# Kernel optimization log

Measured on AMD Instinct MI355X. Metric: run time of the kernel, lower is better.

## Reference

```python
import jax, jax.numpy as jnp
import numpy as np

N_QUBITS = 12
N_LAYERS = 4
BATCH = 1024


def _apply_1q(state, G, w, n):
    # state: (b, 2**n) complex; G: (2,2) shared or (b,2,2) batched gate on wire w
    b = state.shape[0]
    st = state.reshape(b, 2**w, 2, 2**(n - w - 1))
    if G.ndim == 3:
        out = jnp.einsum('bij,bljr->blir', G, st)
    else:
        out = jnp.einsum('ij,bljr->blir', G, st)
    return out.reshape(b, -1)


def _apply_cnot(state, c, t, n):
    # CNOT with control c, target t; reshape so both wire axes are explicit
    b = state.shape[0]
    q0, q1 = (c, t) if c < t else (t, c)
    st = state.reshape(b, 2**q0, 2, 2**(q1 - q0 - 1), 2, 2**(n - q1 - 1))
    if c < t:
        # control axis = 2; flip target axis in the control=1 slice
        out = jnp.stack([st[:, :, 0], jnp.flip(st[:, :, 1], axis=3)], axis=2)
    else:
        # control axis = 4; target axis sits at position 2 of the slice
        out = jnp.stack([st[:, :, :, :, 0], jnp.flip(st[:, :, :, :, 1], axis=2)], axis=4)
    return out.reshape(b, -1)


def _vqc_forward(x, weights):
    b, n = x.shape
    L = weights.shape[0]
    state = jnp.zeros((b, 2**n), jnp.complex64).at[:, 0].set(1.0)
    # AngleEmbedding (default rotation='X'): RX(x[:, w]) on wire w, batched gates
    half = x.astype(jnp.float32) * 0.5
    c, s = jnp.cos(half), jnp.sin(half)
    for w in range(n):
        G = jnp.stack([jnp.stack([c[:, w] + 0j, -1j * s[:, w]], -1),
                       jnp.stack([-1j * s[:, w], c[:, w] + 0j], -1)], -2)  # (b,2,2)
        state = _apply_1q(state, G, w, n)
    # StronglyEntanglingLayers: per layer, Rot(phi,theta,omega) on each wire,
    # then ring of CNOTs with range r = l % (n-1) + 1
    for l in range(L):
        for w in range(n):
            phi, theta, omega = weights[l, w, 0], weights[l, w, 1], weights[l, w, 2]
            ct, sn = jnp.cos(theta * 0.5), jnp.sin(theta * 0.5)
            ep = jnp.exp(0.5j * (phi + omega))
            em = jnp.exp(-0.5j * (phi + omega))
            ed = jnp.exp(0.5j * (phi - omega))
            edc = jnp.exp(-0.5j * (phi - omega))
            # Rot = RZ(omega) @ RY(theta) @ RZ(phi)
            G = jnp.stack([jnp.stack([em * ct, -ed * sn]),
                           jnp.stack([edc * sn, ep * ct])])  # (2,2)
            state = _apply_1q(state, G, w, n)
        r = l % (n - 1) + 1
        for w in range(n):
            state = _apply_cnot(state, w, (w + r) % n, n)
    # <Z_w> = sum over basis states of probs * (+1 if bit w == 0 else -1)
    probs = state.real**2 + state.imag**2
    evs = []
    for w in range(n):
        p = probs.reshape(b, 2**w, 2, -1)
        evs.append(p[:, :, 0, :].sum(axis=(1, 2)) - p[:, :, 1, :].sum(axis=(1, 2)))
    return jnp.stack(evs, axis=1)  # (b, n_qubits)


def setup_inputs() -> dict:
    key = jax.random.key(0)
    k1, k2 = jax.random.split(key)
    x = jax.random.uniform(k1, (BATCH, N_QUBITS), jnp.float32) * np.float32(np.pi)
    weights = jax.random.normal(k2, (N_LAYERS, N_QUBITS, 3), jnp.float32)
    return {"x": x, "weights": weights}


def reference(x, weights):
    return _vqc_forward(x, weights)
```

## Files before the change

kernel.cpp:

```cpp
#include <hip/hip_runtime.h>

#define NQ 12
#define NL 4
typedef __attribute__((ext_vector_type(2))) float f32x2;


__device__ __forceinline__ f32x2 cmul(f32x2 a, f32x2 b) {
    f32x2 r; r.x = a.x*b.x - a.y*b.y; r.y = a.x*b.y + a.y*b.x; return r;
}

__device__ __forceinline__ int SW(int i) {
    return i ^ ((((i >> 4) ^ (i >> 8)) & 7) << 1);
}

template<int P>
__device__ __forceinline__ void ry16(f32x2 (&v)[16], float ct, float sn) {
#pragma unroll
    for (int r0 = 0; r0 < 16; ++r0) {
        if (!(r0 & (1 << P))) {
            const int r1 = r0 | (1 << P);
            const f32x2 a0 = v[r0], a1 = v[r1];
            v[r0] = ct*a0 - sn*a1;
            v[r1] = sn*a0 + ct*a1;
        }
    }
}

__device__ __forceinline__ void ry4grp(f32x2 (&v)[16], const f32x2* rc) {
    const f32x2 c0 = rc[0], c1 = rc[1], c2 = rc[2], c3 = rc[3];
    ry16<3>(v, c0.x, c0.y);
    ry16<2>(v, c1.x, c1.y);
    ry16<1>(v, c2.x, c2.y);
    ry16<0>(v, c3.x, c3.y);
}

__device__ __forceinline__ void diag16(f32x2 (&v)[16], const f32x2* tab, f32x2 tc) {
#pragma unroll
    for (int r = 0; r < 16; ++r)
        v[r] = cmul(v[r], cmul(tc, tab[r]));
}

__device__ constexpr int foldG(int rho, int r) {
    int g = 0;
    if (rho == 1) {
        if (r & 1) g ^= 0xC01; if (r & 2) g ^= 0x003;
        if (r & 4) g ^= 0x006; if (r & 8) g ^= 0x00C;
    } else if (rho == 2) {
        if (r & 1) g ^= 0x501; if (r & 2) g ^= 0xA02;
        if (r & 4) g ^= 0x005; if (r & 8) g ^= 0x00A;
    } else {
        if (r & 1) g ^= 0x241; if (r & 2) g ^= 0x482;
        if (r & 4) g ^= 0x904; if (r & 8) g ^= 0x009;
    }
    return g;
}

template<int RHO>
__device__ __forceinline__ void readCA(f32x2 (&v)[16], const f32x2* buf, int t) {
    int F;
    if constexpr (RHO == 1) F = (t << 4) ^ ((t & 127) << 3) ^ ((t >> 7) << 10);
    else if constexpr (RHO == 2) F = (t << 4) ^ ((t & 255) << 2);
    else F = (t << 4) ^ ((t & 255) << 1);
#pragma unroll
    for (int r = 0; r < 16; ++r)
        v[r] = buf[SW(F ^ foldG(RHO, r))];
}

__global__ __launch_bounds__(256) void vqc_kernel(
    const float* __restrict__ x,
    const float* __restrict__ wts,
    float* __restrict__ out)
{
    __shared__ alignas(16) f32x2 buf[4096];
    __shared__ alignas(16) f32x2 dtabP[NL][16];
    __shared__ alignas(16) f32x2 dtabW[3][16];
    __shared__ alignas(16) f32x2 rcs[NL * NQ];
    __shared__ float wtsL[NL * NQ * 3];
    __shared__ float red[4][NQ];

    const int t = threadIdx.x;
    const int b = blockIdx.x;

    if (t < NL * NQ * 3) wtsL[t] = wts[t];
    if (t < 112) {
        const int tb = t >> 4, e = t & 15;
        float ang = 0.f;
        if (tb < NL) {
#pragma unroll
            for (int j = 0; j < 4; ++j)
                ang += (((e >> j) & 1) ? 0.5f : -0.5f) * wts[(tb*NQ + (11-j))*3 + 0];
            float s, c; __sincosf(ang, &s, &c);
            f32x2 tv = {c, s}; dtabP[tb][e] = tv;
        } else {
            const int l = tb - NL;
#pragma unroll
            for (int j = 0; j < 4; ++j)
                ang += (((e >> j) & 1) ? 0.5f : -0.5f) * wts[(l*NQ + (3-j))*3 + 2];
            float s, c; __sincosf(ang, &s, &c);
            f32x2 tv = {c, s}; dtabW[l][e] = tv;
        }
    }
    if (t < NL * NQ) {
        float s, c; __sincosf(0.5f * wts[t*3 + 1], &s, &c);
        f32x2 tv = {c, s}; rcs[t] = tv;
    }
    __syncthreads();

    float cw[NQ], sw[NQ];
#pragma unroll
    for (int w = 0; w < NQ; ++w)
        __sincosf(0.5f * x[b*NQ + w], &sw[w], &cw[w]);
    float lm = 1.f;
#pragma unroll
    for (int k = 0; k < 8; ++k)
        lm *= ((t >> k) & 1) ? sw[7-k] : cw[7-k];
    const int pt = __popc(t) & 3;
    float pre[4], pim[4];
#pragma unroll
    for (int q = 0; q < 4; ++q) {
        const int kk = (pt + q) & 3;
        pre[q] = (kk == 0) ? 1.f : ((kk == 2) ? -1.f : 0.f);
        pim[q] = (kk == 1) ? -1.f : ((kk == 3) ? 1.f : 0.f);
    }
    f32x2 v[16];
#pragma unroll
    for (int r = 0; r < 16; ++r) {
        float m = lm;
        m *= (r & 1) ? sw[11] : cw[11];
        m *= (r & 2) ? sw[10] : cw[10];
        m *= (r & 4) ? sw[9]  : cw[9];
        m *= (r & 8) ? sw[8]  : cw[8];
        const int pc = __popc(r) & 3;
        v[r].x = m * pre[pc];
        v[r].y = m * pim[pc];
    }

#pragma unroll 1
    for (int l = 0; l < NL; ++l) {
        float angP = 0.f;
#pragma unroll
        for (int k = 0; k < 8; ++k)
            angP += (((t >> k) & 1) ? 0.5f : -0.5f) * wtsL[(l*NQ + (7-k))*3 + 0];
        float sp, cp; __sincosf(angP, &sp, &cp);
        f32x2 tcP = {cp, sp};
        diag16(v, dtabP[l], tcP);

        ry4grp(v, &rcs[l*NQ + 8]);

        __syncthreads();
        {
            float4* b4 = (float4*)buf;
            const int base = t << 4;
#pragma unroll
            for (int r = 0; r < 16; r += 2) {
                const int a = SW(base | r);
                b4[a >> 1] = make_float4(v[r].x, v[r].y, v[r+1].x, v[r+1].y);
            }
        }
        __syncthreads();
        {
            const int hi = (t & 0xF0) << 4, lo = t & 15;
#pragma unroll
            for (int r = 0; r < 16; ++r)
                v[r] = buf[SW(hi | (r << 4) | lo)];
        }

        ry4grp(v, &rcs[l*NQ + 4]);

        __syncthreads();
        {
            const int hi = (t & 0xF0) << 4, lo = t & 15;
#pragma unroll
            for (int r = 0; r < 16; ++r)
                buf[SW(hi | (r << 4) | lo)] = v[r];
        }
        __syncthreads();
#pragma unroll
        for (int r = 0; r < 16; ++r)
            v[r] = buf[SW((r << 8) | t)];

        ry4grp(v, &rcs[l*NQ + 0]);

        if (l == NL - 1) break;

        float angW = 0.f;
#pragma unroll
        for (int k = 0; k < 8; ++k)
            angW += (((t >> k) & 1) ? 0.5f : -0.5f) * wtsL[(l*NQ + (11-k))*3 + 2];
        float so, co; __sincosf(angW, &so, &co);
        f32x2 tcW = {co, so};
        diag16(v, dtabW[l], tcW);

        __syncthreads();
#pragma unroll
        for (int r = 0; r < 16; ++r)
            buf[SW((r << 8) | t)] = v[r];
        __syncthreads();
        if (l == 0)      readCA<1>(v, buf, t);
        else if (l == 1) readCA<2>(v, buf, t);
        else             readCA<3>(v, buf, t);
    }

    float S0 = 0.f, S8 = 0.f, S4 = 0.f, S2 = 0.f, S1 = 0.f;
#pragma unroll
    for (int r = 0; r < 16; ++r) {
        const float p = v[r].x*v[r].x + v[r].y*v[r].y;
        S0 += p;
        S8 += (r & 8) ? -p : p;
        S4 += (r & 4) ? -p : p;
        S2 += (r & 2) ? -p : p;
        S1 += (r & 1) ? -p : p;
    }
    const float g88 = (__popc(t & 0x88) & 1) ? -1.f : 1.f;
    const float g44 = (__popc(t & 0x44) & 1) ? -1.f : 1.f;
    const float g22 = (__popc(t & 0x22) & 1) ? -1.f : 1.f;
    const float g11 = (__popc(t & 0x11) & 1) ? -1.f : 1.f;
    const float g80 = (t & 0x80) ? -1.f : 1.f;
    const float g40 = (t & 0x40) ? -1.f : 1.f;
    const float g20 = (t & 0x20) ? -1.f : 1.f;
    const float g10 = (t & 0x10) ? -1.f : 1.f;

    float ev[NQ];
    ev[0] = g88 * S0;  ev[1] = g44 * S0;  ev[2]  = g22 * S0;  ev[3]  = g11 * S0;
    ev[4] = g80 * S8;  ev[5] = g40 * S4;  ev[6]  = g20 * S2;  ev[7]  = g10 * S1;
    ev[8] = g88 * S8;  ev[9] = g44 * S4;  ev[10] = g22 * S2;  ev[11] = g11 * S1;

#pragma unroll
    for (int w = 0; w < NQ; ++w)
#pragma unroll
        for (int off = 32; off; off >>= 1)
            ev[w] += __shfl_xor(ev[w], off, 64);
    if ((t & 63) == 0) {
#pragma unroll
        for (int w = 0; w < NQ; ++w) red[t >> 6][w] = ev[w];
    }
    __syncthreads();
    if (t < NQ) out[b*NQ + t] = red[0][t] + red[1][t] + red[2][t] + red[3][t];
}

extern "C" void kernel_launch(void* const* d_in, const int* in_sizes, int n_in,
                              void* d_out, int out_size, void* d_ws, size_t ws_size,
                              hipStream_t stream) {
    const float* x   = (const float*)d_in[0];
    const float* wts = (const float*)d_in[1];
    float* out = (float*)d_out;
    const int nb = in_sizes[0] / NQ;
    vqc_kernel<<<dim3(nb), dim3(256), 0, stream>>>(x, wts, out);
}
```

Baseline: 43.10 us.

## Process two batch samples per block and factor RZ diagonal into per-bit phases

Each block now simulates two batch elements with one shared 4096-entry LDS buffer, so the per-block weight setup is amortized and the two state vectors' gate arithmetic can interleave. The 16-entry diagonal phase tables are replaced by four per-bit phase factors plus a scalar offset, applied as successive complex multiplies. Weights are read directly from global memory instead of being staged in shared memory. In exchange there are twice as many barriers per block (serialized permutes through one buffer), higher register pressure from two 16-element complex arrays, half as many blocks, and an odd batch size would drop the last sample.

```diff
diff --git a/kernel.cpp b/kernel.cpp
--- a/kernel.cpp
+++ b/kernel.cpp
@@ -34,10 +34,18 @@
     ry16<0>(v, c3.x, c3.y);
 }
 
-__device__ __forceinline__ void diag16(f32x2 (&v)[16], const f32x2* tab, f32x2 tc) {
-#pragma unroll
-    for (int r = 0; r < 16; ++r)
-        v[r] = cmul(v[r], cmul(tc, tab[r]));
+__device__ __forceinline__ void diag_rz(f32x2 (&v)[16], f32x2 tc, const f32x2* fz) {
+    const f32x2 f0 = fz[0], f1 = fz[1], f2 = fz[2], f3 = fz[3];
+#pragma unroll
+    for (int r = 0; r < 16; ++r) v[r] = cmul(v[r], tc);
+#pragma unroll
+    for (int r = 8; r < 16; ++r) v[r] = cmul(v[r], f0);
+#pragma unroll
+    for (int r = 0; r < 16; ++r) if (r & 4) v[r] = cmul(v[r], f1);
+#pragma unroll
+    for (int r = 0; r < 16; ++r) if (r & 2) v[r] = cmul(v[r], f2);
+#pragma unroll
+    for (int r = 0; r < 16; ++r) if (r & 1) v[r] = cmul(v[r], f3);
 }
 
 __device__ constexpr int foldG(int rho, int r) {
@@ -66,54 +74,41 @@
         v[r] = buf[SW(F ^ foldG(RHO, r))];
 }
 
-__global__ __launch_bounds__(256) void vqc_kernel(
-    const float* __restrict__ x,
-    const float* __restrict__ wts,
-    float* __restrict__ out)
-{
-    __shared__ alignas(16) f32x2 buf[4096];
-    __shared__ alignas(16) f32x2 dtabP[NL][16];
-    __shared__ alignas(16) f32x2 dtabW[3][16];
-    __shared__ alignas(16) f32x2 rcs[NL * NQ];
-    __shared__ float wtsL[NL * NQ * 3];
-    __shared__ float red[4][NQ];
-
-    const int t = threadIdx.x;
-    const int b = blockIdx.x;
-
-    if (t < NL * NQ * 3) wtsL[t] = wts[t];
-    if (t < 112) {
-        const int tb = t >> 4, e = t & 15;
-        float ang = 0.f;
-        if (tb < NL) {
-#pragma unroll
-            for (int j = 0; j < 4; ++j)
-                ang += (((e >> j) & 1) ? 0.5f : -0.5f) * wts[(tb*NQ + (11-j))*3 + 0];
-            float s, c; __sincosf(ang, &s, &c);
-            f32x2 tv = {c, s}; dtabP[tb][e] = tv;
-        } else {
-            const int l = tb - NL;
-#pragma unroll
-            for (int j = 0; j < 4; ++j)
-                ang += (((e >> j) & 1) ? 0.5f : -0.5f) * wts[(l*NQ + (3-j))*3 + 2];
-            float s, c; __sincosf(ang, &s, &c);
-            f32x2 tv = {c, s}; dtabW[l][e] = tv;
-        }
-    }
-    if (t < NL * NQ) {
-        float s, c; __sincosf(0.5f * wts[t*3 + 1], &s, &c);
-        f32x2 tv = {c, s}; rcs[t] = tv;
-    }
-    __syncthreads();
-
+__device__ __forceinline__ void permA_write(const f32x2 (&v)[16], f32x2* buf, int t) {
+    float4* b4 = (float4*)buf;
+    const int base = t << 4;
+#pragma unroll
+    for (int r = 0; r < 16; r += 2) {
+        const int a = SW(base | r);
+        b4[a >> 1] = make_float4(v[r].x, v[r].y, v[r+1].x, v[r+1].y);
+    }
+}
+__device__ __forceinline__ void permB_read(f32x2 (&v)[16], const f32x2* buf, int t) {
+    const int hi = (t & 0xF0) << 4, lo = t & 15;
+#pragma unroll
+    for (int r = 0; r < 16; ++r) v[r] = buf[SW(hi | (r << 4) | lo)];
+}
+__device__ __forceinline__ void permB_write(const f32x2 (&v)[16], f32x2* buf, int t) {
+    const int hi = (t & 0xF0) << 4, lo = t & 15;
+#pragma unroll
+    for (int r = 0; r < 16; ++r) buf[SW(hi | (r << 4) | lo)] = v[r];
+}
+__device__ __forceinline__ void permC_read(f32x2 (&v)[16], const f32x2* buf, int t) {
+#pragma unroll
+    for (int r = 0; r < 16; ++r) v[r] = buf[SW((r << 8) | t)];
+}
+__device__ __forceinline__ void permC_write(const f32x2 (&v)[16], f32x2* buf, int t) {
+#pragma unroll
+    for (int r = 0; r < 16; ++r) buf[SW((r << 8) | t)] = v[r];
+}
+
+__device__ __forceinline__ void embed(f32x2 (&v)[16], const float* __restrict__ xr, int t) {
     float cw[NQ], sw[NQ];
 #pragma unroll
-    for (int w = 0; w < NQ; ++w)
-        __sincosf(0.5f * x[b*NQ + w], &sw[w], &cw[w]);
+    for (int w = 0; w < NQ; ++w) __sincosf(0.5f * xr[w], &sw[w], &cw[w]);
     float lm = 1.f;
 #pragma unroll
-    for (int k = 0; k < 8; ++k)
-        lm *= ((t >> k) & 1) ? sw[7-k] : cw[7-k];
+    for (int k = 0; k < 8; ++k) lm *= ((t >> k) & 1) ? sw[7-k] : cw[7-k];
     const int pt = __popc(t) & 3;
     float pre[4], pim[4];
 #pragma unroll
@@ -122,7 +117,6 @@
         pre[q] = (kk == 0) ? 1.f : ((kk == 2) ? -1.f : 0.f);
         pim[q] = (kk == 1) ? -1.f : ((kk == 3) ? 1.f : 0.f);
     }
-    f32x2 v[16];
 #pragma unroll
     for (int r = 0; r < 16; ++r) {
         float m = lm;
@@ -134,73 +128,9 @@
         v[r].x = m * pre[pc];
         v[r].y = m * pim[pc];
     }
-
-#pragma unroll 1
-    for (int l = 0; l < NL; ++l) {
-        float angP = 0.f;
-#pragma unroll
-        for (int k = 0; k < 8; ++k)
-            angP += (((t >> k) & 1) ? 0.5f : -0.5f) * wtsL[(l*NQ + (7-k))*3 + 0];
-        float sp, cp; __sincosf(angP, &sp, &cp);
-        f32x2 tcP = {cp, sp};
-        diag16(v, dtabP[l], tcP);
-
-        ry4grp(v, &rcs[l*NQ + 8]);
-
-        __syncthreads();
-        {
-            float4* b4 = (float4*)buf;
-            const int base = t << 4;
-#pragma unroll
-            for (int r = 0; r < 16; r += 2) {
-                const int a = SW(base | r);
-                b4[a >> 1] = make_float4(v[r].x, v[r].y, v[r+1].x, v[r+1].y);
-            }
-        }
-        __syncthreads();
-        {
-            const int hi = (t & 0xF0) << 4, lo = t & 15;
-#pragma unroll
-            for (int r = 0; r < 16; ++r)
-                v[r] = buf[SW(hi | (r << 4) | lo)];
-        }
-
-        ry4grp(v, &rcs[l*NQ + 4]);
-
-        __syncthreads();
-        {
-            const int hi = (t & 0xF0) << 4, lo = t & 15;
-#pragma unroll
-            for (int r = 0; r < 16; ++r)
-                buf[SW(hi | (r << 4) | lo)] = v[r];
-        }
-        __syncthreads();
-#pragma unroll
-        for (int r = 0; r < 16; ++r)
-            v[r] = buf[SW((r << 8) | t)];
-
-        ry4grp(v, &rcs[l*NQ + 0]);
-
-        if (l == NL - 1) break;
-
-        float angW = 0.f;
-#pragma unroll
-        for (int k = 0; k < 8; ++k)
-            angW += (((t >> k) & 1) ? 0.5f : -0.5f) * wtsL[(l*NQ + (11-k))*3 + 2];
-        float so, co; __sincosf(angW, &so, &co);
-        f32x2 tcW = {co, so};
-        diag16(v, dtabW[l], tcW);
-
-        __syncthreads();
-#pragma unroll
-        for (int r = 0; r < 16; ++r)
-            buf[SW((r << 8) | t)] = v[r];
-        __syncthreads();
-        if (l == 0)      readCA<1>(v, buf, t);
-        else if (l == 1) readCA<2>(v, buf, t);
-        else             readCA<3>(v, buf, t);
-    }
-
+}
+
+__device__ __forceinline__ void meas(const f32x2 (&v)[16], float (&ev)[NQ], int t) {
     float S0 = 0.f, S8 = 0.f, S4 = 0.f, S2 = 0.f, S1 = 0.f;
 #pragma unroll
     for (int r = 0; r < 16; ++r) {
@@ -219,23 +149,131 @@
     const float g40 = (t & 0x40) ? -1.f : 1.f;
     const float g20 = (t & 0x20) ? -1.f : 1.f;
     const float g10 = (t & 0x10) ? -1.f : 1.f;
-
-    float ev[NQ];
     ev[0] = g88 * S0;  ev[1] = g44 * S0;  ev[2]  = g22 * S0;  ev[3]  = g11 * S0;
     ev[4] = g80 * S8;  ev[5] = g40 * S4;  ev[6]  = g20 * S2;  ev[7]  = g10 * S1;
     ev[8] = g88 * S8;  ev[9] = g44 * S4;  ev[10] = g22 * S2;  ev[11] = g11 * S1;
-
-#pragma unroll
-    for (int w = 0; w < NQ; ++w)
-#pragma unroll
-        for (int off = 32; off; off >>= 1)
-            ev[w] += __shfl_xor(ev[w], off, 64);
+}
+
+__global__ __launch_bounds__(256) void vqc_kernel(
+    const float* __restrict__ x,
+    const float* __restrict__ wts,
+    float* __restrict__ out)
+{
+    __shared__ alignas(16) f32x2 buf[4096];
+    __shared__ alignas(16) f32x2 rcs[NL * NQ];
+    __shared__ alignas(16) f32x2 rzP[NL][4];
+    __shared__ alignas(16) f32x2 rzW[3][4];
+    __shared__ float offs[8];
+    __shared__ float red[2][4][NQ];
+
+    const int t  = threadIdx.x;
+    const int b0 = blockIdx.x * 2, b1 = b0 + 1;
+
+    if (t < NL * NQ) {
+        float s, c; __sincosf(0.5f * wts[t*3 + 1], &s, &c);
+        f32x2 tv = {c, s}; rcs[t] = tv;
+    } else if (t < 64) {
+        const int u = t - 48, l = u >> 2, j = u & 3;
+        float s, c; __sincosf(wts[(l*NQ + 8 + j)*3 + 0], &s, &c);
+        f32x2 tv = {c, s}; rzP[l][j] = tv;
+    } else if (t < 76) {
+        const int u = t - 64, l = u >> 2, j = u & 3;
+        float s, c; __sincosf(wts[(l*NQ + j)*3 + 2], &s, &c);
+        f32x2 tv = {c, s}; rzW[l][j] = tv;
+    } else if (t < 80) {
+        const int l = t - 76;
+        float s = 0.f;
+#pragma unroll
+        for (int j = 0; j < 4; ++j) s += wts[(l*NQ + 8 + j)*3 + 0];
+        offs[l] = -0.5f * s;
+    } else if (t < 83) {
+        const int l = t - 80;
+        float s = 0.f;
+#pragma unroll
+        for (int j = 0; j < 4; ++j) s += wts[(l*NQ + j)*3 + 2];
+        offs[4 + l] = -0.5f * s;
+    }
+
+    f32x2 v0[16], v1[16];
+    embed(v0, x + b0*NQ, t);
+    embed(v1, x + b1*NQ, t);
+    __syncthreads();
+
+#pragma unroll 1
+    for (int l = 0; l < NL; ++l) {
+        float aP = offs[l];
+#pragma unroll
+        for (int k = 0; k < 8; ++k)
+            aP += (((t >> k) & 1) ? 0.5f : -0.5f) * wts[(l*NQ + (7-k))*3 + 0];
+        float sp, cp; __sincosf(aP, &sp, &cp);
+        f32x2 tcP = {cp, sp};
+        diag_rz(v0, tcP, rzP[l]);
+        diag_rz(v1, tcP, rzP[l]);
+        ry4grp(v0, &rcs[l*NQ + 8]);
+        ry4grp(v1, &rcs[l*NQ + 8]);
+
+        __syncthreads(); permA_write(v0, buf, t);
+        __syncthreads(); permB_read(v0, buf, t);
+        __syncthreads(); permA_write(v1, buf, t);
+        __syncthreads(); permB_read(v1, buf, t);
+        ry4grp(v0, &rcs[l*NQ + 4]);
+        ry4grp(v1, &rcs[l*NQ + 4]);
+
+        __syncthreads(); permB_write(v0, buf, t);
+        __syncthreads(); permC_read(v0, buf, t);
+        __syncthreads(); permB_write(v1, buf, t);
+        __syncthreads(); permC_read(v1, buf, t);
+        ry4grp(v0, &rcs[l*NQ + 0]);
+        ry4grp(v1, &rcs[l*NQ + 0]);
+
+        if (l == NL - 1) break;
+
+        float aW = offs[4 + l];
+#pragma unroll
+        for (int k = 0; k < 8; ++k)
+            aW += (((t >> k) & 1) ? 0.5f : -0.5f) * wts[(l*NQ + (11-k))*3 + 2];
+        float so, co; __sincosf(aW, &so, &co);
+        f32x2 tcW = {co, so};
+        diag_rz(v0, tcW, rzW[l]);
+        diag_rz(v1, tcW, rzW[l]);
+
+        __syncthreads(); permC_write(v0, buf, t);
+        __syncthreads();
+        if (l == 0)      readCA<1>(v0, buf, t);
+        else if (l == 1) readCA<2>(v0, buf, t);
+        else             readCA<3>(v0, buf, t);
+        __syncthreads(); permC_write(v1, buf, t);
+        __syncthreads();
+        if (l == 0)      readCA<1>(v1, buf, t);
+        else if (l == 1) readCA<2>(v1, buf, t);
+        else             readCA<3>(v1, buf, t);
+    }
+
+    float ev0[NQ], ev1[NQ];
+    meas(v0, ev0, t);
+    meas(v1, ev1, t);
+#pragma unroll
+    for (int w = 0; w < NQ; ++w) {
+#pragma unroll
+        for (int off = 32; off; off >>= 1) {
+            ev0[w] += __shfl_xor(ev0[w], off, 64);
+            ev1[w] += __shfl_xor(ev1[w], off, 64);
+        }
+    }
     if ((t & 63) == 0) {
 #pragma unroll
-        for (int w = 0; w < NQ; ++w) red[t >> 6][w] = ev[w];
+        for (int w = 0; w < NQ; ++w) {
+            red[0][t >> 6][w] = ev0[w];
+            red[1][t >> 6][w] = ev1[w];
+        }
     }
     __syncthreads();
-    if (t < NQ) out[b*NQ + t] = red[0][t] + red[1][t] + red[2][t] + red[3][t];
+    if (t < NQ)
+        out[b0*NQ + t] = red[0][0][t] + red[0][1][t] + red[0][2][t] + red[0][3][t];
+    else if (t >= 64 && t < 64 + NQ) {
+        const int w = t - 64;
+        out[b1*NQ + w] = red[1][0][w] + red[1][1][w] + red[1][2][w] + red[1][3][w];
+    }
 }
 
 extern "C" void kernel_launch(void* const* d_in, const int* in_sizes, int n_in,
@@ -244,6 +282,6 @@
     const float* x   = (const float*)d_in[0];
     const float* wts = (const float*)d_in[1];
     float* out = (float*)d_out;
-    const int nb = in_sizes[0] / NQ;
-    vqc_kernel<<<dim3(nb), dim3(256), 0, stream>>>(x, wts, out);
-}
+    const int nb2 = (in_sizes[0] / NQ) / 2;
+    vqc_kernel<<<dim3(nb2), dim3(256), 0, stream>>>(x, wts, out);
+}
```

After: 53.49 us. 1.24x slower.

## Halve block to 128 threads with 32 amplitudes each, DPP gate and fused CNOT exchange

Applied to the files above, without the earlier changes.

Each block now uses 128 threads holding 32 amplitudes per thread instead of 256 holding 16, so five wires are applied in registers per pass. One wire's rotation is done through a cross-lane DPP swap, and the CNOT ring permutation is fused with the next rotation during the shared-memory read. This cuts the number of shared-memory transposes and barriers per layer, and one barrier is replaced by a local lgkmcnt wait that relies on the write/read mapping staying within a wavefront. In exchange, register pressure rises and there are fewer threads per block.

```diff
diff --git a/kernel.cpp b/kernel.cpp
--- a/kernel.cpp
+++ b/kernel.cpp
@@ -9,14 +9,19 @@
     f32x2 r; r.x = a.x*b.x - a.y*b.y; r.y = a.x*b.y + a.y*b.x; return r;
 }
 
-__device__ __forceinline__ int SW(int i) {
-    return i ^ ((((i >> 4) ^ (i >> 8)) & 7) << 1);
+__host__ __device__ constexpr int SLc(int s) {
+    return s ^ ((((s >> 5) ^ (s >> 9)) & 15) << 1);
+}
+
+__device__ __forceinline__ float dppx1(float x) {
+    return __int_as_float(__builtin_amdgcn_mov_dpp(__float_as_int(x), 0xB1, 0xF, 0xF, true));
 }
 
 template<int P>
-__device__ __forceinline__ void ry16(f32x2 (&v)[16], float ct, float sn) {
-#pragma unroll
-    for (int r0 = 0; r0 < 16; ++r0) {
+__device__ __forceinline__ void ry32(f32x2 (&v)[32], f32x2 g) {
+    const float ct = g.x, sn = g.y;
+#pragma unroll
+    for (int r0 = 0; r0 < 32; ++r0) {
         if (!(r0 & (1 << P))) {
             const int r1 = r0 | (1 << P);
             const f32x2 a0 = v[r0], a1 = v[r1];
@@ -26,95 +31,124 @@
     }
 }
 
-__device__ __forceinline__ void ry4grp(f32x2 (&v)[16], const f32x2* rc) {
-    const f32x2 c0 = rc[0], c1 = rc[1], c2 = rc[2], c3 = rc[3];
-    ry16<3>(v, c0.x, c0.y);
-    ry16<2>(v, c1.x, c1.y);
-    ry16<1>(v, c2.x, c2.y);
-    ry16<0>(v, c3.x, c3.y);
-}
-
-__device__ __forceinline__ void diag16(f32x2 (&v)[16], const f32x2* tab, f32x2 tc) {
-#pragma unroll
-    for (int r = 0; r < 16; ++r)
-        v[r] = cmul(v[r], cmul(tc, tab[r]));
-}
-
-__device__ constexpr int foldG(int rho, int r) {
+__device__ __forceinline__ void diag32(f32x2 (&v)[32], f32x2 tc, const f32x2* f) {
+#pragma unroll
+    for (int r = 0; r < 32; ++r) v[r] = cmul(v[r], tc);
+#pragma unroll
+    for (int j = 0; j < 5; ++j) {
+        const f32x2 fj = f[j];
+#pragma unroll
+        for (int r = 0; r < 32; ++r)
+            if (r & (1 << j)) v[r] = cmul(v[r], fj);
+    }
+}
+
+template<int RHO>
+__device__ __forceinline__ constexpr int GmaskF(int r) {
     int g = 0;
-    if (rho == 1) {
-        if (r & 1) g ^= 0xC01; if (r & 2) g ^= 0x003;
-        if (r & 4) g ^= 0x006; if (r & 8) g ^= 0x00C;
-    } else if (rho == 2) {
-        if (r & 1) g ^= 0x501; if (r & 2) g ^= 0xA02;
-        if (r & 4) g ^= 0x005; if (r & 8) g ^= 0x00A;
+    if constexpr (RHO == 1) {
+        if (r & 1) g ^= 0xC01; if (r & 2) g ^= 0x003; if (r & 4) g ^= 0x006;
+        if (r & 8) g ^= 0x00C; if (r & 16) g ^= 0x018;
+        if ((r ^ (r >> 1)) & 1) g ^= 0x41;
+    } else if constexpr (RHO == 2) {
+        if (r & 1) g ^= 0x501; if (r & 2) g ^= 0xA02; if (r & 4) g ^= 0x005;
+        if (r & 8) g ^= 0x00A; if (r & 16) g ^= 0x014;
+        if ((r ^ (r >> 2)) & 1) g ^= 0x41;
     } else {
-        if (r & 1) g ^= 0x241; if (r & 2) g ^= 0x482;
-        if (r & 4) g ^= 0x904; if (r & 8) g ^= 0x009;
-    }
-    return g;
+        if (r & 1) g ^= 0x241; if (r & 2) g ^= 0x482; if (r & 4) g ^= 0x904;
+        if (r & 8) g ^= 0x009; if (r & 16) g ^= 0x012;
+        if ((r >> 3) & 1) g ^= 0x41;
+    }
+    return SLc(g);
 }
 
 template<int RHO>
-__device__ __forceinline__ void readCA(f32x2 (&v)[16], const f32x2* buf, int t) {
-    int F;
-    if constexpr (RHO == 1) F = (t << 4) ^ ((t & 127) << 3) ^ ((t >> 7) << 10);
-    else if constexpr (RHO == 2) F = (t << 4) ^ ((t & 255) << 2);
-    else F = (t << 4) ^ ((t & 255) << 1);
-#pragma unroll
-    for (int r = 0; r < 16; ++r)
-        v[r] = buf[SW(F ^ foldG(RHO, r))];
-}
-
-__global__ __launch_bounds__(256) void vqc_kernel(
+__device__ __forceinline__ void exchange_ring(f32x2 (&v)[32], const f32x2* buf, int t,
+    f32x2 cAa, f32x2 cBa, f32x2 cAb, f32x2 cBb)
+{
+    int T = 0;
+    if constexpr (RHO == 1) {
+        if (t & 64) T ^= 0xC00; if (t & 32) T ^= 0x600; if (t & 16) T ^= 0x300;
+        if (t & 8) T ^= 0x180;  if (t & 4) T ^= 0x0C0;  if (t & 2) T ^= 0x060;
+        if (t & 1) T ^= 0x030;
+        if (((t >> 1) ^ (t >> 2)) & 1) T ^= 0x41;
+    } else if constexpr (RHO == 2) {
+        if (t & 64) T ^= 0xA00; if (t & 32) T ^= 0x500; if (t & 16) T ^= 0x280;
+        if (t & 8) T ^= 0x140;  if (t & 4) T ^= 0x0A0;  if (t & 2) T ^= 0x050;
+        if (t & 1) T ^= 0x028;
+        if (((t >> 1) ^ (t >> 3)) & 1) T ^= 0x41;
+    } else {
+        if (t & 64) T ^= 0x900; if (t & 32) T ^= 0x480; if (t & 16) T ^= 0x240;
+        if (t & 8) T ^= 0x120;  if (t & 4) T ^= 0x090;  if (t & 2) T ^= 0x048;
+        if (t & 1) T ^= 0x024;
+        if (((t >> 1) ^ (t >> 4)) & 1) T ^= 0x41;
+    }
+    const int TT = SLc(T);
+#pragma unroll
+    for (int r = 0; r < 32; ++r) {
+        const int s0 = TT ^ GmaskF<RHO>(r);
+        const f32x2 a  = buf[s0];
+        const f32x2 bb = buf[s0 ^ 0x808];
+        const bool hb = (r >> (RHO - 1)) & 1;
+        const f32x2 cA = hb ? cAb : cAa;
+        const f32x2 cB = hb ? cBb : cBa;
+        v[r] = cmul(cA, a) + cmul(cB, bb);
+    }
+}
+
+__global__ __launch_bounds__(128) void vqc_kernel(
     const float* __restrict__ x,
     const float* __restrict__ wts,
     float* __restrict__ out)
 {
     __shared__ alignas(16) f32x2 buf[4096];
-    __shared__ alignas(16) f32x2 dtabP[NL][16];
-    __shared__ alignas(16) f32x2 dtabW[3][16];
     __shared__ alignas(16) f32x2 rcs[NL * NQ];
-    __shared__ float wtsL[NL * NQ * 3];
-    __shared__ float red[4][NQ];
+    __shared__ alignas(16) f32x2 fphi[NL][5];
+    __shared__ alignas(16) f32x2 fomg[3][5];
+    __shared__ f32x2 eo[3];
+    __shared__ float offp[NL], offo[3];
+    __shared__ float red[2][NQ];
 
     const int t = threadIdx.x;
     const int b = blockIdx.x;
 
-    if (t < NL * NQ * 3) wtsL[t] = wts[t];
-    if (t < 112) {
-        const int tb = t >> 4, e = t & 15;
-        float ang = 0.f;
-        if (tb < NL) {
-#pragma unroll
-            for (int j = 0; j < 4; ++j)
-                ang += (((e >> j) & 1) ? 0.5f : -0.5f) * wts[(tb*NQ + (11-j))*3 + 0];
-            float s, c; __sincosf(ang, &s, &c);
-            f32x2 tv = {c, s}; dtabP[tb][e] = tv;
-        } else {
-            const int l = tb - NL;
-#pragma unroll
-            for (int j = 0; j < 4; ++j)
-                ang += (((e >> j) & 1) ? 0.5f : -0.5f) * wts[(l*NQ + (3-j))*3 + 2];
-            float s, c; __sincosf(ang, &s, &c);
-            f32x2 tv = {c, s}; dtabW[l][e] = tv;
-        }
-    }
-    if (t < NL * NQ) {
+    if (t < 48) {
         float s, c; __sincosf(0.5f * wts[t*3 + 1], &s, &c);
         f32x2 tv = {c, s}; rcs[t] = tv;
-    }
-    __syncthreads();
+    } else if (t < 68) {
+        const int u = t - 48, l = u / 5, j = u % 5;
+        float s, c; __sincosf(wts[(l*NQ + 11 - j)*3 + 0], &s, &c);
+        f32x2 tv = {c, s}; fphi[l][j] = tv;
+    } else if (t < 83) {
+        const int u = t - 68, l = u / 5, j = u % 5;
+        float s, c; __sincosf(wts[(l*NQ + 5 - j)*3 + 2], &s, &c);
+        f32x2 tv = {c, s}; fomg[l][j] = tv;
+    } else if (t < 86) {
+        const int l = t - 83;
+        float s, c; __sincosf(0.5f * wts[(l*NQ + 0)*3 + 2], &s, &c);
+        f32x2 tv = {c, s}; eo[l] = tv;
+    } else if (t < 90) {
+        const int l = t - 86;
+        float s = 0.f;
+#pragma unroll
+        for (int w = 7; w <= 11; ++w) s += wts[(l*NQ + w)*3 + 0];
+        offp[l] = -0.5f * s;
+    } else if (t < 93) {
+        const int l = t - 90;
+        float s = 0.f;
+#pragma unroll
+        for (int w = 1; w <= 5; ++w) s += wts[(l*NQ + w)*3 + 2];
+        offo[l] = -0.5f * s;
+    }
 
     float cw[NQ], sw[NQ];
 #pragma unroll
-    for (int w = 0; w < NQ; ++w)
-        __sincosf(0.5f * x[b*NQ + w], &sw[w], &cw[w]);
+    for (int w = 0; w < NQ; ++w) __sincosf(0.5f * x[b*NQ + w], &sw[w], &cw[w]);
     float lm = 1.f;
 #pragma unroll
-    for (int k = 0; k < 8; ++k)
-        lm *= ((t >> k) & 1) ? sw[7-k] : cw[7-k];
-    const int pt = __popc(t) & 3;
+    for (int k = 0; k < 7; ++k)
+        lm *= ((t >> k) & 1) ? sw[6-k] : cw[6-k];
+    const int pt = __popc(t & 127) & 3;
     float pre[4], pim[4];
 #pragma unroll
     for (int q = 0; q < 4; ++q) {
@@ -122,108 +156,148 @@
         pre[q] = (kk == 0) ? 1.f : ((kk == 2) ? -1.f : 0.f);
         pim[q] = (kk == 1) ? -1.f : ((kk == 3) ? 1.f : 0.f);
     }
-    f32x2 v[16];
-#pragma unroll
-    for (int r = 0; r < 16; ++r) {
+    f32x2 v[32];
+#pragma unroll
+    for (int r = 0; r < 32; ++r) {
         float m = lm;
-        m *= (r & 1) ? sw[11] : cw[11];
-        m *= (r & 2) ? sw[10] : cw[10];
-        m *= (r & 4) ? sw[9]  : cw[9];
-        m *= (r & 8) ? sw[8]  : cw[8];
+        m *= (r & 1)  ? sw[11] : cw[11];
+        m *= (r & 2)  ? sw[10] : cw[10];
+        m *= (r & 4)  ? sw[9]  : cw[9];
+        m *= (r & 8)  ? sw[8]  : cw[8];
+        m *= (r & 16) ? sw[7]  : cw[7];
         const int pc = __popc(r) & 3;
         v[r].x = m * pre[pc];
         v[r].y = m * pim[pc];
     }
+    __syncthreads();
+
+    const int wA = (t << 5) ^ (((t ^ (t >> 4)) & 15) << 1);
+    const int jb = ((t & 64) << 5) | ((t & 1) << 5) | ((t >> 1) & 31);
+    const int rbase = SLc(jb);
+    const int wbase = SLc(jb ^ (((t >> 1) & 1) ? 0x41 : 0));
+    float4* const b4 = (float4*)buf;
 
 #pragma unroll 1
     for (int l = 0; l < NL; ++l) {
-        float angP = 0.f;
-#pragma unroll
-        for (int k = 0; k < 8; ++k)
-            angP += (((t >> k) & 1) ? 0.5f : -0.5f) * wtsL[(l*NQ + (7-k))*3 + 0];
-        float sp, cp; __sincosf(angP, &sp, &cp);
-        f32x2 tcP = {cp, sp};
-        diag16(v, dtabP[l], tcP);
-
-        ry4grp(v, &rcs[l*NQ + 8]);
-
-        __syncthreads();
         {
-            float4* b4 = (float4*)buf;
-            const int base = t << 4;
-#pragma unroll
-            for (int r = 0; r < 16; r += 2) {
-                const int a = SW(base | r);
-                b4[a >> 1] = make_float4(v[r].x, v[r].y, v[r+1].x, v[r+1].y);
-            }
-        }
-        __syncthreads();
+            float ang = offp[l];
+#pragma unroll
+            for (int k = 0; k < 7; ++k) {
+                const float a = 0.5f * wts[(l*NQ + (6-k))*3 + 0];
+                ang += ((t >> k) & 1) ? a : -a;
+            }
+            float s, c; __sincosf(ang, &s, &c);
+            f32x2 tc = {c, s};
+            diag32(v, tc, fphi[l]);
+        }
+        ry32<4>(v, rcs[l*NQ + 7]);  ry32<3>(v, rcs[l*NQ + 8]);
+        ry32<2>(v, rcs[l*NQ + 9]);  ry32<1>(v, rcs[l*NQ + 10]);
+        ry32<0>(v, rcs[l*NQ + 11]);
+
+#pragma unroll
+        for (int r = 0; r < 32; r += 2) {
+            const int sl = wA ^ r;
+            b4[sl >> 1] = make_float4(v[r].x, v[r].y, v[r+1].x, v[r+1].y);
+        }
+        asm volatile("s_waitcnt lgkmcnt(0)" ::: "memory");
+#pragma unroll
+        for (int r = 0; r < 32; ++r)
+            v[r] = buf[rbase ^ SLc(r << 6)];
+
+        ry32<4>(v, rcs[l*NQ + 1]);  ry32<3>(v, rcs[l*NQ + 2]);
+        ry32<2>(v, rcs[l*NQ + 3]);  ry32<1>(v, rcs[l*NQ + 4]);
+        ry32<0>(v, rcs[l*NQ + 5]);
+
         {
-            const int hi = (t & 0xF0) << 4, lo = t & 15;
-#pragma unroll
-            for (int r = 0; r < 16; ++r)
-                v[r] = buf[SW(hi | (r << 4) | lo)];
-        }
-
-        ry4grp(v, &rcs[l*NQ + 4]);
-
-        __syncthreads();
-        {
-            const int hi = (t & 0xF0) << 4, lo = t & 15;
-#pragma unroll
-            for (int r = 0; r < 16; ++r)
-                buf[SW(hi | (r << 4) | lo)] = v[r];
-        }
-        __syncthreads();
-#pragma unroll
-        for (int r = 0; r < 16; ++r)
-            v[r] = buf[SW((r << 8) | t)];
-
-        ry4grp(v, &rcs[l*NQ + 0]);
-
-        if (l == NL - 1) break;
-
-        float angW = 0.f;
-#pragma unroll
-        for (int k = 0; k < 8; ++k)
-            angW += (((t >> k) & 1) ? 0.5f : -0.5f) * wtsL[(l*NQ + (11-k))*3 + 2];
-        float so, co; __sincosf(angW, &so, &co);
-        f32x2 tcW = {co, so};
-        diag16(v, dtabW[l], tcW);
-
-        __syncthreads();
-#pragma unroll
-        for (int r = 0; r < 16; ++r)
-            buf[SW((r << 8) | t)] = v[r];
-        __syncthreads();
-        if (l == 0)      readCA<1>(v, buf, t);
-        else if (l == 1) readCA<2>(v, buf, t);
-        else             readCA<3>(v, buf, t);
-    }
-
-    float S0 = 0.f, S8 = 0.f, S4 = 0.f, S2 = 0.f, S1 = 0.f;
-#pragma unroll
-    for (int r = 0; r < 16; ++r) {
+            const f32x2 g = rcs[l*NQ + 6];
+            const float ct = g.x;
+            const float sB = (t & 1) ? g.y : -g.y;
+#pragma unroll
+            for (int r = 0; r < 32; ++r) {
+                f32x2 y; y.x = dppx1(v[r].x); y.y = dppx1(v[r].y);
+                v[r] = ct * v[r] + sB * y;
+            }
+        }
+
+        if (l < NL - 1) {
+            {
+                float ang = offo[l];
+                float a;
+                a = 0.5f*wts[(l*NQ + 6)*3 + 2];  ang += (t & 1)  ? a : -a;
+                a = 0.5f*wts[(l*NQ + 7)*3 + 2];  ang += (t & 32) ? a : -a;
+                a = 0.5f*wts[(l*NQ + 8)*3 + 2];  ang += (t & 16) ? a : -a;
+                a = 0.5f*wts[(l*NQ + 9)*3 + 2];  ang += (t & 8)  ? a : -a;
+                a = 0.5f*wts[(l*NQ + 10)*3 + 2]; ang += (t & 4)  ? a : -a;
+                a = 0.5f*wts[(l*NQ + 11)*3 + 2]; ang += (t & 2)  ? a : -a;
+                float s, c; __sincosf(ang, &s, &c);
+                f32x2 tc = {c, s};
+                diag32(v, tc, fomg[l]);
+            }
+#pragma unroll
+            for (int r = 0; r < 32; r += 2) {
+                const int sl = wbase ^ SLc(r << 6);
+                b4[sl >> 1] = make_float4(v[r].x, v[r].y, v[r+1].x, v[r+1].y);
+            }
+            __syncthreads();
+            {
+                const f32x2 g0 = rcs[l*NQ + 0];
+                const float ct = g0.x, sn = g0.y;
+                const f32x2 e = eo[l];
+                f32x2 em = {e.x, -e.y}, ep = e;
+                f32x2 cA0 = ct*em, cB0 = -sn*em;
+                f32x2 cA1 = ct*ep, cB1 =  sn*ep;
+                const bool t6 = (t >> 6) & 1;
+                const f32x2 cAa = t6 ? cA1 : cA0, cBa = t6 ? cB1 : cB0;
+                const f32x2 cAb = t6 ? cA0 : cA1, cBb = t6 ? cB0 : cB1;
+                if (l == 0)      exchange_ring<1>(v, buf, t, cAa, cBa, cAb, cBb);
+                else if (l == 1) exchange_ring<2>(v, buf, t, cAa, cBa, cAb, cBb);
+                else             exchange_ring<3>(v, buf, t, cAa, cBa, cAb, cBb);
+            }
+            __syncthreads();
+        } else {
+#pragma unroll
+            for (int r = 0; r < 32; r += 2) {
+                const int sl = wbase ^ SLc(r << 6);
+                b4[sl >> 1] = make_float4(v[r].x, v[r].y, v[r+1].x, v[r+1].y);
+            }
+            __syncthreads();
+            const f32x2 g0 = rcs[l*NQ + 0];
+            const float ct = g0.x;
+            const float sB = (t & 64) ? g0.y : -g0.y;
+#pragma unroll
+            for (int r = 0; r < 32; r += 2) {
+                const int sl = (wbase ^ SLc(r << 6)) ^ 0x808;
+                const float4 q = b4[sl >> 1];
+                f32x2 p0 = {q.x, q.y}, p1 = {q.z, q.w};
+                v[r]   = ct * v[r]   + sB * p0;
+                v[r+1] = ct * v[r+1] + sB * p1;
+            }
+        }
+    }
+
+    float S0=0, R0=0, R1=0, R2=0, R3=0, R40=0;
+#pragma unroll
+    for (int r = 0; r < 32; ++r) {
         const float p = v[r].x*v[r].x + v[r].y*v[r].y;
         S0 += p;
-        S8 += (r & 8) ? -p : p;
-        S4 += (r & 4) ? -p : p;
-        S2 += (r & 2) ? -p : p;
-        S1 += (r & 1) ? -p : p;
-    }
-    const float g88 = (__popc(t & 0x88) & 1) ? -1.f : 1.f;
-    const float g44 = (__popc(t & 0x44) & 1) ? -1.f : 1.f;
-    const float g22 = (__popc(t & 0x22) & 1) ? -1.f : 1.f;
-    const float g11 = (__popc(t & 0x11) & 1) ? -1.f : 1.f;
-    const float g80 = (t & 0x80) ? -1.f : 1.f;
-    const float g40 = (t & 0x40) ? -1.f : 1.f;
-    const float g20 = (t & 0x20) ? -1.f : 1.f;
-    const float g10 = (t & 0x10) ? -1.f : 1.f;
+        R0  += (r & 1) ? -p : p;
+        R1  += (r & 2) ? -p : p;
+        R2  += (r & 4) ? -p : p;
+        R3  += (r & 8) ? -p : p;
+        R40 += (((r >> 4) ^ r) & 1) ? -p : p;
+    }
+    const float st0 = (t & 1)  ? -1.f : 1.f;
+    const float st1 = (t & 2)  ? -1.f : 1.f;
+    const float st2 = (t & 4)  ? -1.f : 1.f;
+    const float st3 = (t & 8)  ? -1.f : 1.f;
+    const float st4 = (t & 16) ? -1.f : 1.f;
+    const float st5 = (t & 32) ? -1.f : 1.f;
+    const float st6 = (t & 64) ? -1.f : 1.f;
 
     float ev[NQ];
-    ev[0] = g88 * S0;  ev[1] = g44 * S0;  ev[2]  = g22 * S0;  ev[3]  = g11 * S0;
-    ev[4] = g80 * S8;  ev[5] = g40 * S4;  ev[6]  = g20 * S2;  ev[7]  = g10 * S1;
-    ev[8] = g88 * S8;  ev[9] = g44 * S4;  ev[10] = g22 * S2;  ev[11] = g11 * S1;
+    ev[0] = R1*st4;      ev[1] = R0*st3;      ev[2]  = S0*st0*st2;  ev[3]  = S0*st5*st1;
+    ev[4] = R1*st6;      ev[5] = R40;         ev[6]  = R3*st0;      ev[7]  = R2*st5;
+    ev[8] = R1*st6*st4;  ev[9] = R40*st3;     ev[10] = R3*st0*st2;  ev[11] = R2*st5*st1;
 
 #pragma unroll
     for (int w = 0; w < NQ; ++w)
@@ -235,7 +309,7 @@
         for (int w = 0; w < NQ; ++w) red[t >> 6][w] = ev[w];
     }
     __syncthreads();
-    if (t < NQ) out[b*NQ + t] = red[0][t] + red[1][t] + red[2][t] + red[3][t];
+    if (t < NQ) out[b*NQ + t] = red[0][t] + red[1][t];
 }
 
 extern "C" void kernel_launch(void* const* d_in, const int* in_sizes, int n_in,
@@ -245,5 +319,5 @@
     const float* wts = (const float*)d_in[1];
     float* out = (float*)d_out;
     const int nb = in_sizes[0] / NQ;
-    vqc_kernel<<<dim3(nb), dim3(256), 0, stream>>>(x, wts, out);
-}
+    vqc_kernel<<<dim3(nb), dim3(128), 0, stream>>>(x, wts, out);
+}
```

New measurement: 62.38 us, median of 4. 44.7% more time.
